# Performance work log

Measured on AMD Instinct MI355X. Metric: run time of the kernel, lower is better.

## Reference

```python
import jax, jax.numpy as jnp
import numpy as np

D_MODEL = 1024
NUM_HEADS = 16
DEPTH = D_MODEL // NUM_HEADS


def setup_inputs() -> dict:
    key = jax.random.key(0)
    ks = jax.random.split(key, 9)
    s = 1.0 / np.sqrt(D_MODEL)
    return {
        "inputs": jax.random.normal(ks[0], (2, 2048, D_MODEL), dtype=jnp.float32),
        "wq": jax.random.normal(ks[1], (D_MODEL, D_MODEL), dtype=jnp.float32) * s,
        "bq": jnp.zeros((D_MODEL,), dtype=jnp.float32),
        "wk": jax.random.normal(ks[2], (D_MODEL, D_MODEL), dtype=jnp.float32) * s,
        "bk": jnp.zeros((D_MODEL,), dtype=jnp.float32),
        "wv": jax.random.normal(ks[3], (D_MODEL, D_MODEL), dtype=jnp.float32) * s,
        "bv": jnp.zeros((D_MODEL,), dtype=jnp.float32),
        "wo": jax.random.normal(ks[4], (D_MODEL, D_MODEL), dtype=jnp.float32) * s,
        "bo": jnp.zeros((D_MODEL,), dtype=jnp.float32),
    }


def _split_heads(x, B, S):
    # [B, S, d_model] -> [B, H, S, depth]
    return x.reshape(B, S, NUM_HEADS, DEPTH).transpose(0, 2, 1, 3)


def reference(inputs, wq, bq, wk, bk, wv, bv, wo, bo):
    B, S, _ = inputs.shape
    q = _split_heads(inputs @ wq + bq, B, S)
    k = _split_heads(inputs @ wk + bk, B, S)
    v = _split_heads(inputs @ wv + bv, B, S)
    scale = 1.0 / jnp.sqrt(jnp.asarray(DEPTH, dtype=inputs.dtype))
    logits = jnp.einsum("bhqd,bhkd->bhqk", q, k) * scale
    attn = jax.nn.softmax(logits, axis=-1)  # [B, H, S, S]
    ctx = jnp.einsum("bhqk,bhkd->bhqd", attn, v)
    ctx = ctx.transpose(0, 2, 1, 3).reshape(B, S, D_MODEL)
    out = ctx @ wo + bo
    return out, attn
```

## Files before the change

### kernel.cpp

```cpp
#include <hip/hip_runtime.h>

typedef _Float16 f16;
typedef _Float16 f16x8 __attribute__((ext_vector_type(8)));
typedef _Float16 f16x4 __attribute__((ext_vector_type(4)));
typedef float f32x4 __attribute__((ext_vector_type(4)));

#define MFMA16(a, b, c) __builtin_amdgcn_mfma_f32_16x16x32_f16((a), (b), (c), 0, 0, 0)

constexpr int DM = 1024;
constexpr int NH = 16;
constexpr int DEPTH = 64;
constexpr int SEQ = 2048;
constexpr int BATCH = 2;
constexpr int MTOT = BATCH * SEQ;

__device__ __forceinline__ int swzA(int row, int off) {
  return row * 64 + (off ^ ((row & 7) << 3));
}
__device__ __forceinline__ int swzG(int row, int off) {
  return row * 32 + (off ^ (((row >> 1) & 3) << 3));
}

__global__ void k_cvt(const float* __restrict__ x, f16* __restrict__ y, int n) {
  int i = (blockIdx.x * blockDim.x + threadIdx.x) * 4;
  if (i >= n) return;
  const float4 v = *(const float4*)(x + i);
  f16x4 h;
  h[0] = (f16)v.x; h[1] = (f16)v.y; h[2] = (f16)v.z; h[3] = (f16)v.w;
  *(f16x4*)(y + i) = h;
}

template <int FINAL>
__global__ __launch_bounds__(256, 3) void k_gemm(const f16* __restrict__ A,
                                                 const float* __restrict__ B0,
                                                 const float* __restrict__ B1,
                                                 const float* __restrict__ B2,
                                                 const float* __restrict__ bias0,
                                                 const float* __restrict__ bias1,
                                                 const float* __restrict__ bias2,
                                                 void* __restrict__ o0,
                                                 void* __restrict__ o1,
                                                 void* __restrict__ o2) {
  constexpr int K = DM, N = DM;
  __shared__ f16 Al[128 * 32];
  __shared__ f16 Bl[128 * 32];
  const int z = blockIdx.z;
  const float* Bw   = FINAL ? B0 : (z == 0 ? B0 : (z == 1 ? B1 : B2));
  const float* bias = FINAL ? bias0 : (z == 0 ? bias0 : (z == 1 ? bias1 : bias2));
  void* outp        = FINAL ? o0 : (z == 0 ? o0 : (z == 1 ? o1 : o2));
  const int mode = FINAL ? 1 : (z == 2 ? 2 : 0);

  const int tid = threadIdx.x;
  const int lane = tid & 63;
  const int wave = tid >> 6;
  const int m0 = blockIdx.y * 128;
  const int n0 = blockIdx.x * 128;
  const int wr = (wave >> 1) * 64;
  const int wc = (wave & 1) * 64;
  const int lr = lane & 15;
  const int lk = (lane >> 4) * 8;

  f32x4 acc[4][4];
  for (int i = 0; i < 4; i++)
    for (int j = 0; j < 4; j++) acc[i][j] = (f32x4)0.0f;

  const int ar = tid >> 1, ak = (tid & 1) * 16;
  const int bn = (tid & 31) * 4, bk = (tid >> 5) * 4;

  f16x8 a0r, a1r;
  float4 w0, w1, w2, w3;
  {
    const f16* ag = A + (size_t)(m0 + ar) * K + ak;
    a0r = *(const f16x8*)(ag);
    a1r = *(const f16x8*)(ag + 8);
    const float* bg = Bw + (size_t)bk * N + n0 + bn;
    w0 = *(const float4*)(bg);
    w1 = *(const float4*)(bg + N);
    w2 = *(const float4*)(bg + 2 * N);
    w3 = *(const float4*)(bg + 3 * N);
  }

  for (int k0 = 0; k0 < K; k0 += 32) {
    __syncthreads();
    *(f16x8*)(Al + swzG(ar, ak))     = a0r;
    *(f16x8*)(Al + swzG(ar, ak + 8)) = a1r;
    for (int j = 0; j < 4; j++) {
      f16x4 h;
      h[0] = (f16)(((const float*)&w0)[j]);
      h[1] = (f16)(((const float*)&w1)[j]);
      h[2] = (f16)(((const float*)&w2)[j]);
      h[3] = (f16)(((const float*)&w3)[j]);
      *(f16x4*)(Bl + swzG(bn + j, bk)) = h;
    }
    __syncthreads();
    if (k0 + 32 < K) {
      const f16* ag = A + (size_t)(m0 + ar) * K + (k0 + 32) + ak;
      a0r = *(const f16x8*)(ag);
      a1r = *(const f16x8*)(ag + 8);
      const float* bg = Bw + (size_t)(k0 + 32 + bk) * N + n0 + bn;
      w0 = *(const float4*)(bg);
      w1 = *(const float4*)(bg + N);
      w2 = *(const float4*)(bg + 2 * N);
      w3 = *(const float4*)(bg + 3 * N);
    }
    f16x8 af[4], bf[4];
    for (int i = 0; i < 4; i++)
      af[i] = *(const f16x8*)(Al + swzG(wr + i * 16 + lr, lk));
    for (int j = 0; j < 4; j++)
      bf[j] = *(const f16x8*)(Bl + swzG(wc + j * 16 + lr, lk));
    for (int i = 0; i < 4; i++)
      for (int j = 0; j < 4; j++) acc[i][j] = MFMA16(af[i], bf[j], acc[i][j]);
  }

  for (int j = 0; j < 4; j++) {
    const int n = n0 + wc + j * 16 + lr;
    const float bv = bias[n];
    for (int i = 0; i < 4; i++) {
      for (int r = 0; r < 4; r++) {
        const int m = m0 + wr + i * 16 + (lane >> 4) * 4 + r;
        const float val = acc[i][j][r] + bv;
        if (mode == 1) {
          ((float*)outp)[(size_t)m * N + n] = val;
        } else {
          const int b = m >> 11, s = m & 2047;
          const int h = n >> 6, d = n & 63;
          size_t idx;
          if (mode == 0)
            idx = ((size_t)(b * NH + h) * SEQ + s) * DEPTH + d;
          else
            idx = ((size_t)(b * NH + h) * DEPTH + d) * SEQ + s;
          ((f16*)outp)[idx] = (f16)val;
        }
      }
    }
  }
}

__global__ __launch_bounds__(256) void k_attn(const f16* __restrict__ qws,
                                              const f16* __restrict__ kws,
                                              const f16* __restrict__ vtws,
                                              float* __restrict__ attn,
                                              f16* __restrict__ ctx) {
  __shared__ f16 Qs[64 * 64];
  __shared__ f16 Ks[64 * 64];
  __shared__ f16 Vs[64 * 64];
  __shared__ f16 Ps[4][16 * 64];

  const int tid = threadIdx.x, lane = tid & 63, wave = tid >> 6;
  const int bh = blockIdx.y;
  const int q0 = blockIdx.x * 64;
  const int lr = lane & 15, g = lane >> 4, lk = g * 8;

  const f16* qb = qws + (size_t)bh * SEQ * DEPTH;
  const f16* kb = kws + (size_t)bh * SEQ * DEPTH;
  const f16* vb = vtws + (size_t)bh * DEPTH * SEQ;

  const int sr = tid >> 2, sc = (tid & 3) * 16;
  {
    const f16* qg = qb + (size_t)(q0 + sr) * 64 + sc;
    *(f16x8*)(Qs + swzA(sr, sc))     = *(const f16x8*)(qg);
    *(f16x8*)(Qs + swzA(sr, sc + 8)) = *(const f16x8*)(qg + 8);
  }
  __syncthreads();
  const f16x8 qf0 = *(const f16x8*)(Qs + swzA(wave * 16 + lr, lk));
  const f16x8 qf1 = *(const f16x8*)(Qs + swzA(wave * 16 + lr, 32 + lk));

  f16x8 kr0, kr1;
  {
    const f16* kg = kb + (size_t)sr * 64 + sc;
    kr0 = *(const f16x8*)(kg);
    kr1 = *(const f16x8*)(kg + 8);
  }
  float rsum = 0.f;
  for (int kt = 0; kt < SEQ; kt += 64) {
    __syncthreads();
    *(f16x8*)(Ks + swzA(sr, sc))     = kr0;
    *(f16x8*)(Ks + swzA(sr, sc + 8)) = kr1;
    __syncthreads();
    if (kt + 64 < SEQ) {
      const f16* kg = kb + (size_t)(kt + 64 + sr) * 64 + sc;
      kr0 = *(const f16x8*)(kg);
      kr1 = *(const f16x8*)(kg + 8);
    }
    for (int nb = 0; nb < 4; nb++) {
      f32x4 a = (f32x4)0.0f;
      f16x8 kf0 = *(const f16x8*)(Ks + swzA(nb * 16 + lr, lk));
      f16x8 kf1 = *(const f16x8*)(Ks + swzA(nb * 16 + lr, 32 + lk));
      a = MFMA16(kf0, qf0, a);
      a = MFMA16(kf1, qf1, a);
      rsum += (__expf(a[0] * 0.125f) + __expf(a[1] * 0.125f)) +
              (__expf(a[2] * 0.125f) + __expf(a[3] * 0.125f));
    }
  }
  rsum += __shfl_xor(rsum, 16);
  rsum += __shfl_xor(rsum, 32);
  const float rsinv = 1.0f / rsum;

  f32x4 cacc[4];
  for (int d = 0; d < 4; d++) cacc[d] = (f32x4)0.0f;
  float* ab = attn + (size_t)bh * SEQ * SEQ + (size_t)(q0 + wave * 16 + lr) * SEQ + g * 4;

  f16x8 vr0, vr1;
  {
    const f16* kg = kb + (size_t)sr * 64 + sc;
    kr0 = *(const f16x8*)(kg);
    kr1 = *(const f16x8*)(kg + 8);
    const f16* vg = vb + (size_t)sr * SEQ + sc;
    vr0 = *(const f16x8*)(vg);
    vr1 = *(const f16x8*)(vg + 8);
  }
  f16* Psw = Ps[wave];

  for (int kt = 0; kt < SEQ; kt += 64) {
    __syncthreads();
    *(f16x8*)(Ks + swzA(sr, sc))     = kr0;
    *(f16x8*)(Ks + swzA(sr, sc + 8)) = kr1;
    *(f16x8*)(Vs + swzA(sr, sc))     = vr0;
    *(f16x8*)(Vs + swzA(sr, sc + 8)) = vr1;
    __syncthreads();
    if (kt + 64 < SEQ) {
      const f16* kg = kb + (size_t)(kt + 64 + sr) * 64 + sc;
      kr0 = *(const f16x8*)(kg);
      kr1 = *(const f16x8*)(kg + 8);
      const f16* vg = vb + (size_t)sr * SEQ + kt + 64 + sc;
      vr0 = *(const f16x8*)(vg);
      vr1 = *(const f16x8*)(vg + 8);
    }
    for (int nb = 0; nb < 4; nb++) {
      f32x4 a = (f32x4)0.0f;
      f16x8 kf0 = *(const f16x8*)(Ks + swzA(nb * 16 + lr, lk));
      f16x8 kf1 = *(const f16x8*)(Ks + swzA(nb * 16 + lr, 32 + lk));
      a = MFMA16(kf0, qf0, a);
      a = MFMA16(kf1, qf1, a);
      const float p0 = __expf(a[0] * 0.125f) * rsinv;
      const float p1 = __expf(a[1] * 0.125f) * rsinv;
      const float p2 = __expf(a[2] * 0.125f) * rsinv;
      const float p3 = __expf(a[3] * 0.125f) * rsinv;
      f32x4 pq;
      pq[0] = p0; pq[1] = p1; pq[2] = p2; pq[3] = p3;
      __builtin_nontemporal_store(pq, (f32x4*)(ab + kt + nb * 16));
      f16x4 ph;
      ph[0] = (f16)p0; ph[1] = (f16)p1; ph[2] = (f16)p2; ph[3] = (f16)p3;
      *(f16x4*)(Psw + swzA(lr, nb * 16 + g * 4)) = ph;
    }
    __syncthreads();
    for (int ks = 0; ks < 2; ks++) {
      f16x8 pf = *(const f16x8*)(Psw + swzA(lr, ks * 32 + lk));
      for (int d = 0; d < 4; d++) {
        f16x8 vf = *(const f16x8*)(Vs + swzA(d * 16 + lr, ks * 32 + lk));
        cacc[d] = MFMA16(pf, vf, cacc[d]);
      }
    }
  }

  const int b = bh >> 4, h = bh & 15;
  for (int d = 0; d < 4; d++) {
    for (int r = 0; r < 4; r++) {
      const int qrow = q0 + wave * 16 + g * 4 + r;
      ctx[(size_t)(b * SEQ + qrow) * DM + h * DEPTH + d * 16 + lr] = (f16)cacc[d][r];
    }
  }
}

extern "C" void kernel_launch(void* const* d_in, const int* in_sizes, int n_in,
                              void* d_out, int out_size, void* d_ws, size_t ws_size,
                              hipStream_t stream) {
  const float* X  = (const float*)d_in[0];
  const float* wq = (const float*)d_in[1];
  const float* bq = (const float*)d_in[2];
  const float* wk = (const float*)d_in[3];
  const float* bk = (const float*)d_in[4];
  const float* wv = (const float*)d_in[5];
  const float* bv = (const float*)d_in[6];
  const float* wo = (const float*)d_in[7];
  const float* bo = (const float*)d_in[8];

  char* ws = (char*)d_ws;
  f16* Xh  = (f16*)(ws);
  f16* Qw  = (f16*)(ws + ((size_t)8 << 20));
  f16* Kw  = (f16*)(ws + ((size_t)16 << 20));
  f16* Vw  = (f16*)(ws + ((size_t)24 << 20));
  f16* Ctx = (f16*)(ws + ((size_t)32 << 20));

  float* out  = (float*)d_out;
  float* attn = out + (size_t)MTOT * DM;

  k_cvt<<<dim3(MTOT * DM / 1024), dim3(256), 0, stream>>>(X, Xh, MTOT * DM);
  k_gemm<0><<<dim3(DM / 128, MTOT / 128, 3), 256, 0, stream>>>(
      Xh, wq, wk, wv, bq, bk, bv, (void*)Qw, (void*)Kw, (void*)Vw);
  k_attn<<<dim3(SEQ / 64, BATCH * NH), 256, 0, stream>>>(Qw, Kw, Vw, attn, Ctx);
  k_gemm<1><<<dim3(DM / 128, MTOT / 128, 1), 256, 0, stream>>>(
      Ctx, wo, wo, wo, bo, bo, bo, (void*)out, (void*)out, (void*)out);
}
```

Before: 766.4 us.

## Load attention K/V fragments directly from global memory, drop LDS staging and barriers

The attention kernel no longer stages Q, K and V tiles through shared memory with block-wide barriers. Each wave reads its MFMA fragments straight from global memory and relies on L1/L2 caching, and the per-wave P buffer is used without a block barrier. Block indices are remapped so that blocks sharing a head are grouped together for cache locality. The V-transpose projection epilogue now writes 4 consecutive f16 values as one vector store instead of four scalar stores. This trades barrier and LDS traffic for redundant global/L2 reads across the four waves.

```diff
diff --git a/kernel.cpp b/kernel.cpp
--- a/kernel.cpp
+++ b/kernel.cpp
@@ -112,24 +112,29 @@
       for (int j = 0; j < 4; j++) acc[i][j] = MFMA16(af[i], bf[j], acc[i][j]);
   }
 
+  const int g = lane >> 4;
   for (int j = 0; j < 4; j++) {
     const int n = n0 + wc + j * 16 + lr;
     const float bv = bias[n];
     for (int i = 0; i < 4; i++) {
-      for (int r = 0; r < 4; r++) {
-        const int m = m0 + wr + i * 16 + (lane >> 4) * 4 + r;
-        const float val = acc[i][j][r] + bv;
-        if (mode == 1) {
-          ((float*)outp)[(size_t)m * N + n] = val;
-        } else {
-          const int b = m >> 11, s = m & 2047;
-          const int h = n >> 6, d = n & 63;
-          size_t idx;
-          if (mode == 0)
-            idx = ((size_t)(b * NH + h) * SEQ + s) * DEPTH + d;
-          else
-            idx = ((size_t)(b * NH + h) * DEPTH + d) * SEQ + s;
-          ((f16*)outp)[idx] = (f16)val;
+      if (mode == 2) {
+        const int m = m0 + wr + i * 16 + g * 4;
+        const int b = m >> 11, s = m & 2047;
+        const int h = n >> 6, d = n & 63;
+        f16x4 hv;
+        for (int r = 0; r < 4; r++) hv[r] = (f16)(acc[i][j][r] + bv);
+        *(f16x4*)((f16*)outp + ((size_t)(b * NH + h) * DEPTH + d) * SEQ + s) = hv;
+      } else {
+        for (int r = 0; r < 4; r++) {
+          const int m = m0 + wr + i * 16 + g * 4 + r;
+          const float val = acc[i][j][r] + bv;
+          if (mode == 1) {
+            ((float*)outp)[(size_t)m * N + n] = val;
+          } else {
+            const int b = m >> 11, s = m & 2047;
+            const int h = n >> 6, d = n & 63;
+            ((f16*)outp)[((size_t)(b * NH + h) * SEQ + s) * DEPTH + d] = (f16)val;
+          }
         }
       }
     }
@@ -141,51 +146,32 @@
                                               const f16* __restrict__ vtws,
                                               float* __restrict__ attn,
                                               f16* __restrict__ ctx) {
-  __shared__ f16 Qs[64 * 64];
-  __shared__ f16 Ks[64 * 64];
-  __shared__ f16 Vs[64 * 64];
   __shared__ f16 Ps[4][16 * 64];
 
   const int tid = threadIdx.x, lane = tid & 63, wave = tid >> 6;
-  const int bh = blockIdx.y;
-  const int q0 = blockIdx.x * 64;
+  const int flat = blockIdx.y * 32 + blockIdx.x;
+  const int swz = (flat & 7) * 128 + (flat >> 3);
+  const int bh = swz >> 5;
+  const int q0 = (swz & 31) * 64;
   const int lr = lane & 15, g = lane >> 4, lk = g * 8;
 
   const f16* qb = qws + (size_t)bh * SEQ * DEPTH;
   const f16* kb = kws + (size_t)bh * SEQ * DEPTH;
   const f16* vb = vtws + (size_t)bh * DEPTH * SEQ;
 
-  const int sr = tid >> 2, sc = (tid & 3) * 16;
-  {
-    const f16* qg = qb + (size_t)(q0 + sr) * 64 + sc;
-    *(f16x8*)(Qs + swzA(sr, sc))     = *(const f16x8*)(qg);
-    *(f16x8*)(Qs + swzA(sr, sc + 8)) = *(const f16x8*)(qg + 8);
-  }
-  __syncthreads();
-  const f16x8 qf0 = *(const f16x8*)(Qs + swzA(wave * 16 + lr, lk));
-  const f16x8 qf1 = *(const f16x8*)(Qs + swzA(wave * 16 + lr, 32 + lk));
-
-  f16x8 kr0, kr1;
-  {
-    const f16* kg = kb + (size_t)sr * 64 + sc;
-    kr0 = *(const f16x8*)(kg);
-    kr1 = *(const f16x8*)(kg + 8);
-  }
+  const f16* qg = qb + (size_t)(q0 + wave * 16 + lr) * 64;
+  const f16x8 qf0 = *(const f16x8*)(qg + lk);
+  const f16x8 qf1 = *(const f16x8*)(qg + 32 + lk);
+
   float rsum = 0.f;
   for (int kt = 0; kt < SEQ; kt += 64) {
-    __syncthreads();
-    *(f16x8*)(Ks + swzA(sr, sc))     = kr0;
-    *(f16x8*)(Ks + swzA(sr, sc + 8)) = kr1;
-    __syncthreads();
-    if (kt + 64 < SEQ) {
-      const f16* kg = kb + (size_t)(kt + 64 + sr) * 64 + sc;
-      kr0 = *(const f16x8*)(kg);
-      kr1 = *(const f16x8*)(kg + 8);
-    }
+    const f16* kp = kb + (size_t)kt * 64;
+#pragma unroll
     for (int nb = 0; nb < 4; nb++) {
+      const f16* kr = kp + (nb * 16 + lr) * 64;
+      f16x8 kf0 = *(const f16x8*)(kr + lk);
+      f16x8 kf1 = *(const f16x8*)(kr + 32 + lk);
       f32x4 a = (f32x4)0.0f;
-      f16x8 kf0 = *(const f16x8*)(Ks + swzA(nb * 16 + lr, lk));
-      f16x8 kf1 = *(const f16x8*)(Ks + swzA(nb * 16 + lr, 32 + lk));
       a = MFMA16(kf0, qf0, a);
       a = MFMA16(kf1, qf1, a);
       rsum += (__expf(a[0] * 0.125f) + __expf(a[1] * 0.125f)) +
@@ -199,37 +185,16 @@
   f32x4 cacc[4];
   for (int d = 0; d < 4; d++) cacc[d] = (f32x4)0.0f;
   float* ab = attn + (size_t)bh * SEQ * SEQ + (size_t)(q0 + wave * 16 + lr) * SEQ + g * 4;
-
-  f16x8 vr0, vr1;
-  {
-    const f16* kg = kb + (size_t)sr * 64 + sc;
-    kr0 = *(const f16x8*)(kg);
-    kr1 = *(const f16x8*)(kg + 8);
-    const f16* vg = vb + (size_t)sr * SEQ + sc;
-    vr0 = *(const f16x8*)(vg);
-    vr1 = *(const f16x8*)(vg + 8);
-  }
   f16* Psw = Ps[wave];
 
   for (int kt = 0; kt < SEQ; kt += 64) {
-    __syncthreads();
-    *(f16x8*)(Ks + swzA(sr, sc))     = kr0;
-    *(f16x8*)(Ks + swzA(sr, sc + 8)) = kr1;
-    *(f16x8*)(Vs + swzA(sr, sc))     = vr0;
-    *(f16x8*)(Vs + swzA(sr, sc + 8)) = vr1;
-    __syncthreads();
-    if (kt + 64 < SEQ) {
-      const f16* kg = kb + (size_t)(kt + 64 + sr) * 64 + sc;
-      kr0 = *(const f16x8*)(kg);
-      kr1 = *(const f16x8*)(kg + 8);
-      const f16* vg = vb + (size_t)sr * SEQ + kt + 64 + sc;
-      vr0 = *(const f16x8*)(vg);
-      vr1 = *(const f16x8*)(vg + 8);
-    }
+    const f16* kp = kb + (size_t)kt * 64;
+#pragma unroll
     for (int nb = 0; nb < 4; nb++) {
+      const f16* kr = kp + (nb * 16 + lr) * 64;
+      f16x8 kf0 = *(const f16x8*)(kr + lk);
+      f16x8 kf1 = *(const f16x8*)(kr + 32 + lk);
       f32x4 a = (f32x4)0.0f;
-      f16x8 kf0 = *(const f16x8*)(Ks + swzA(nb * 16 + lr, lk));
-      f16x8 kf1 = *(const f16x8*)(Ks + swzA(nb * 16 + lr, 32 + lk));
       a = MFMA16(kf0, qf0, a);
       a = MFMA16(kf1, qf1, a);
       const float p0 = __expf(a[0] * 0.125f) * rsinv;
@@ -243,11 +208,12 @@
       ph[0] = (f16)p0; ph[1] = (f16)p1; ph[2] = (f16)p2; ph[3] = (f16)p3;
       *(f16x4*)(Psw + swzA(lr, nb * 16 + g * 4)) = ph;
     }
-    __syncthreads();
+#pragma unroll
     for (int ks = 0; ks < 2; ks++) {
       f16x8 pf = *(const f16x8*)(Psw + swzA(lr, ks * 32 + lk));
+#pragma unroll
       for (int d = 0; d < 4; d++) {
-        f16x8 vf = *(const f16x8*)(Vs + swzA(d * 16 + lr, ks * 32 + lk));
+        f16x8 vf = *(const f16x8*)(vb + (size_t)(d * 16 + lr) * SEQ + kt + ks * 32 + lk);
         cacc[d] = MFMA16(pf, vf, cacc[d]);
       }
     }
```

After: 919.2 us. 19.9% more time.
